# Kernel optimization log

Hardware: AMD Instinct MI355X
Metric: run time of the kernel (lower is better)

The kernel has to match this reference:

```python
import jax, jax.numpy as jnp
import numpy as np

VOCAB, H, HEADS, S, FF = 100, 8, 2, 6, 16
HD = H // HEADS  # head_dim = 4
EPS = 1e-5


def _layernorm(x, g, b):
    mu = jnp.mean(x, axis=-1, keepdims=True)
    var = jnp.mean((x - mu) ** 2, axis=-1, keepdims=True)
    return (x - mu) * jax.lax.rsqrt(var + EPS) * g + b


def setup_inputs() -> dict:
    key = jax.random.key(0)
    ks = jax.random.split(key, 20)
    B = 262144
    d = {
        'input_ids': jax.random.randint(ks[0], (B, S), 0, VOCAB),
        'tok_emb': jax.random.normal(ks[1], (VOCAB, H), jnp.float32) * 0.02,
        'pos_emb': jax.random.normal(ks[2], (S, H), jnp.float32) * 0.02,
        'Wq': jax.random.normal(ks[3], (H, H), jnp.float32) * 0.1,
        'bq': jnp.zeros((H,), jnp.float32),
        'Wk': jax.random.normal(ks[4], (H, H), jnp.float32) * 0.1,
        'bk': jnp.zeros((H,), jnp.float32),
        'Wv': jax.random.normal(ks[5], (H, H), jnp.float32) * 0.1,
        'bv': jnp.zeros((H,), jnp.float32),
        'Wo': jax.random.normal(ks[6], (H, H), jnp.float32) * 0.1,
        'bo': jnp.zeros((H,), jnp.float32),
        'W1': jax.random.normal(ks[7], (FF, H), jnp.float32) * 0.1,
        'b1': jnp.zeros((FF,), jnp.float32),
        'W2': jax.random.normal(ks[8], (H, FF), jnp.float32) * 0.1,
        'b2': jnp.zeros((H,), jnp.float32),
        'g1': jnp.ones((H,), jnp.float32),
        'be1': jnp.zeros((H,), jnp.float32),
        'g2': jnp.ones((H,), jnp.float32),
        'be2': jnp.zeros((H,), jnp.float32),
    }
    return d


def reference(input_ids, tok_emb, pos_emb, Wq, bq, Wk, bk, Wv, bv, Wo, bo,
              W1, b1, W2, b2, g1, be1, g2, be2):
    B, Sq = input_ids.shape
    x = tok_emb[input_ids] + pos_emb[None, :, :]  # [B,S,H]
    q = x @ Wq.T + bq
    k = x @ Wk.T + bk
    v = x @ Wv.T + bv
    # split heads: [B, heads, S, head_dim]
    q = q.reshape(B, Sq, HEADS, HD).transpose(0, 2, 1, 3)
    k = k.reshape(B, Sq, HEADS, HD).transpose(0, 2, 1, 3)
    v = v.reshape(B, Sq, HEADS, HD).transpose(0, 2, 1, 3)
    scores = jnp.einsum('bhsd,bhtd->bhst', q, k) / (HD ** 0.5)
    probs = jax.nn.softmax(scores, axis=-1)
    attn = jnp.einsum('bhst,bhtd->bhsd', probs, v)
    attn = attn.transpose(0, 2, 1, 3).reshape(B, Sq, H)
    attn = attn @ Wo.T + bo
    h = _layernorm(x + attn, g1, be1)
    ffn = jax.nn.gelu(h @ W1.T + b1, approximate=False) @ W2.T + b2
    return _layernorm(h + ffn, g2, be2)
```

## Files before the change

### kernel.cpp

```cpp
#include <hip/hip_runtime.h>

#define TT_S 6
#define TT_H 8
#define TT_FF 16

__global__ __launch_bounds__(256, 3) void tt_fused(
    const int* __restrict__ ids,
    const float* __restrict__ tok_emb, const float* __restrict__ pos_emb,
    const float* __restrict__ Wq, const float* __restrict__ bq,
    const float* __restrict__ Wk, const float* __restrict__ bk,
    const float* __restrict__ Wv, const float* __restrict__ bv,
    const float* __restrict__ Wo, const float* __restrict__ bo,
    const float* __restrict__ W1, const float* __restrict__ b1,
    const float* __restrict__ W2, const float* __restrict__ b2,
    const float* __restrict__ g1, const float* __restrict__ be1,
    const float* __restrict__ g2, const float* __restrict__ be2,
    float* __restrict__ out, int B)
{
  __shared__ __align__(16) float s_tok[800];
  const int tid = threadIdx.x;
  for (int i = tid; i < 800; i += 256) s_tok[i] = tok_emb[i];
  __syncthreads();

  const int b = blockIdx.x * 256 + tid;
  if (b >= B) return;

  const int* idp = ids + (size_t)b * TT_S;
  int2 i0 = *(const int2*)(idp + 0);
  int2 i1 = *(const int2*)(idp + 2);
  int2 i2 = *(const int2*)(idp + 4);
  unsigned long long P =
      (unsigned long long)(unsigned)i0.x        |
      ((unsigned long long)(unsigned)i0.y << 8) |
      ((unsigned long long)(unsigned)i1.x << 16)|
      ((unsigned long long)(unsigned)i1.y << 24)|
      ((unsigned long long)(unsigned)i2.x << 32)|
      ((unsigned long long)(unsigned)i2.y << 40);

  float km[TT_S][TT_H], vm[TT_S][TT_H];
  {
    float x[TT_S][TT_H];
    const int idv[TT_S] = { i0.x, i0.y, i1.x, i1.y, i2.x, i2.y };
    #pragma unroll
    for (int t = 0; t < TT_S; ++t) {
      const float4* tr = (const float4*)(s_tok + idv[t] * TT_H);
      float4 a0 = tr[0];
      float4 a1 = tr[1];
      x[t][0] = a0.x + pos_emb[t*8+0];
      x[t][1] = a0.y + pos_emb[t*8+1];
      x[t][2] = a0.z + pos_emb[t*8+2];
      x[t][3] = a0.w + pos_emb[t*8+3];
      x[t][4] = a1.x + pos_emb[t*8+4];
      x[t][5] = a1.y + pos_emb[t*8+5];
      x[t][6] = a1.z + pos_emb[t*8+6];
      x[t][7] = a1.w + pos_emb[t*8+7];
    }
    #pragma unroll
    for (int i = 0; i < TT_H; ++i) {
      float ak[TT_S], av[TT_S];
      float bki = bk[i], bvi = bv[i];
      #pragma unroll
      for (int t = 0; t < TT_S; ++t) { ak[t] = bki; av[t] = bvi; }
      #pragma unroll
      for (int j = 0; j < TT_H; ++j) {
        float wk = Wk[i*8+j], wv = Wv[i*8+j];
        #pragma unroll
        for (int t = 0; t < TT_S; ++t) {
          ak[t] = fmaf(x[t][j], wk, ak[t]);
          av[t] = fmaf(x[t][j], wv, av[t]);
        }
      }
      #pragma unroll
      for (int t = 0; t < TT_S; ++t) { km[t][i] = ak[t]; vm[t][i] = av[t]; }
    }
  }

  float* op = out + (size_t)b * (TT_S * TT_H);
  #pragma unroll 1
  for (int s = 0; s < TT_S; ++s) {
    const int tok = (int)((P >> (s * 8)) & 0xFF);
    const float4* xr = (const float4*)(s_tok + tok * TT_H);
    float4 a0 = xr[0];
    float4 a1 = xr[1];
    float xs[TT_H];
    xs[0] = a0.x + pos_emb[s*8+0];
    xs[1] = a0.y + pos_emb[s*8+1];
    xs[2] = a0.z + pos_emb[s*8+2];
    xs[3] = a0.w + pos_emb[s*8+3];
    xs[4] = a1.x + pos_emb[s*8+4];
    xs[5] = a1.y + pos_emb[s*8+5];
    xs[6] = a1.z + pos_emb[s*8+6];
    xs[7] = a1.w + pos_emb[s*8+7];

    float qs[TT_H];
    #pragma unroll
    for (int i = 0; i < TT_H; ++i) {
      float a = bq[i];
      #pragma unroll
      for (int j = 0; j < TT_H; ++j) a = fmaf(xs[j], Wq[i*8+j], a);
      qs[i] = a * 0.5f;
    }

    float attn[TT_H];
    #pragma unroll
    for (int hh = 0; hh < 2; ++hh) {
      const int hb = hh * 4;
      float sc[TT_S];
      float sum = 0.f;
      #pragma unroll
      for (int t = 0; t < TT_S; ++t) {
        float d = qs[hb+0] * km[t][hb+0];
        d = fmaf(qs[hb+1], km[t][hb+1], d);
        d = fmaf(qs[hb+2], km[t][hb+2], d);
        d = fmaf(qs[hb+3], km[t][hb+3], d);
        sc[t] = __expf(d);
        sum += sc[t];
      }
      float inv = __builtin_amdgcn_rcpf(sum);
      float a0_ = 0.f, a1_ = 0.f, a2_ = 0.f, a3_ = 0.f;
      #pragma unroll
      for (int t = 0; t < TT_S; ++t) {
        a0_ = fmaf(sc[t], vm[t][hb+0], a0_);
        a1_ = fmaf(sc[t], vm[t][hb+1], a1_);
        a2_ = fmaf(sc[t], vm[t][hb+2], a2_);
        a3_ = fmaf(sc[t], vm[t][hb+3], a3_);
      }
      attn[hb+0] = a0_ * inv;
      attn[hb+1] = a1_ * inv;
      attn[hb+2] = a2_ * inv;
      attn[hb+3] = a3_ * inv;
    }

    float r[TT_H];
    float mu = 0.f;
    #pragma unroll
    for (int i = 0; i < TT_H; ++i) {
      float o = bo[i];
      #pragma unroll
      for (int j = 0; j < TT_H; ++j) o = fmaf(attn[j], Wo[i*8+j], o);
      r[i] = xs[i] + o;
      mu += r[i];
    }
    mu *= 0.125f;
    float var = 0.f;
    #pragma unroll
    for (int i = 0; i < TT_H; ++i) { float d = r[i] - mu; var = fmaf(d, d, var); }
    var *= 0.125f;
    float rin = __builtin_amdgcn_rsqf(var + 1e-5f);
    float hr[TT_H];
    #pragma unroll
    for (int i = 0; i < TT_H; ++i)
      hr[i] = fmaf((r[i] - mu) * rin, g1[i], be1[i]);

    float f1[TT_FF];
    #pragma unroll
    for (int f = 0; f < TT_FF; ++f) {
      float u = b1[f];
      #pragma unroll
      for (int j = 0; j < TT_H; ++j) u = fmaf(hr[j], W1[f*8+j], u);
      float u2 = u * u;
      float p  = fmaf(0.044715f, u2, 1.0f);
      float z2 = fminf(1.5957691216057308f * u * p, 60.f);
      float e  = __expf(z2);
      f1[f] = u * e * __builtin_amdgcn_rcpf(e + 1.0f);
    }

    float r2[TT_H];
    float mu2 = 0.f;
    #pragma unroll
    for (int i = 0; i < TT_H; ++i) {
      float y = b2[i];
      #pragma unroll
      for (int f = 0; f < TT_FF; ++f) y = fmaf(f1[f], W2[i*16+f], y);
      r2[i] = hr[i] + y;
      mu2 += r2[i];
    }
    mu2 *= 0.125f;
    float var2 = 0.f;
    #pragma unroll
    for (int i = 0; i < TT_H; ++i) { float d = r2[i] - mu2; var2 = fmaf(d, d, var2); }
    var2 *= 0.125f;
    float rin2 = __builtin_amdgcn_rsqf(var2 + 1e-5f);
    float res[TT_H];
    #pragma unroll
    for (int i = 0; i < TT_H; ++i)
      res[i] = fmaf((r2[i] - mu2) * rin2, g2[i], be2[i]);

    float4 v0; v0.x = res[0]; v0.y = res[1]; v0.z = res[2]; v0.w = res[3];
    float4 v1; v1.x = res[4]; v1.y = res[5]; v1.z = res[6]; v1.w = res[7];
    ((float4*)(op + s*8))[0] = v0;
    ((float4*)(op + s*8))[1] = v1;
  }
}

extern "C" void kernel_launch(void* const* d_in, const int* in_sizes, int n_in,
                              void* d_out, int out_size, void* d_ws, size_t ws_size,
                              hipStream_t stream) {
  const int*   ids = (const int*)  d_in[0];
  const float* tok = (const float*)d_in[1];
  const float* pos = (const float*)d_in[2];
  const float* Wq  = (const float*)d_in[3];
  const float* bq  = (const float*)d_in[4];
  const float* Wk  = (const float*)d_in[5];
  const float* bk  = (const float*)d_in[6];
  const float* Wv  = (const float*)d_in[7];
  const float* bv  = (const float*)d_in[8];
  const float* Wo  = (const float*)d_in[9];
  const float* bo  = (const float*)d_in[10];
  const float* W1  = (const float*)d_in[11];
  const float* b1  = (const float*)d_in[12];
  const float* W2  = (const float*)d_in[13];
  const float* b2  = (const float*)d_in[14];
  const float* g1  = (const float*)d_in[15];
  const float* be1 = (const float*)d_in[16];
  const float* g2  = (const float*)d_in[17];
  const float* be2 = (const float*)d_in[18];
  float* out = (float*)d_out;

  const int B = in_sizes[0] / TT_S;
  const int grid = (B + 255) / 256;
  hipLaunchKernelGGL(tt_fused, dim3(grid), dim3(256), 0, stream,
                     ids, tok, pos, Wq, bq, Wk, bk, Wv, bv, Wo, bo,
                     W1, b1, W2, b2, g1, be1, g2, be2, out, B);
}
```

Baseline: 166.2 us.

## Map one thread per token and share K/V through LDS

Result: faster. 142.8 us (-14.1%).

```diff
diff --git a/kernel.cpp b/kernel.cpp
--- a/kernel.cpp
+++ b/kernel.cpp
@@ -3,8 +3,11 @@
 #define TT_S 6
 #define TT_H 8
 #define TT_FF 16
-
-__global__ __launch_bounds__(256, 3) void tt_fused(
+#define SEQ_PER_BLK 64
+#define BLK (SEQ_PER_BLK * TT_S)
+#define KV_STRIDE 108
+
+__global__ __launch_bounds__(BLK, 6) void tt_fused(
     const int* __restrict__ ids,
     const float* __restrict__ tok_emb, const float* __restrict__ pos_emb,
     const float* __restrict__ Wq, const float* __restrict__ bq,
@@ -18,178 +21,162 @@
     float* __restrict__ out, int B)
 {
   __shared__ __align__(16) float s_tok[800];
+  __shared__ __align__(16) float s_pos[48];
+  __shared__ __align__(16) float s_kv[SEQ_PER_BLK * KV_STRIDE];
+
   const int tid = threadIdx.x;
-  for (int i = tid; i < 800; i += 256) s_tok[i] = tok_emb[i];
+  for (int i = tid; i < 800; i += BLK) s_tok[i] = tok_emb[i];
+  if (tid < 48) s_pos[tid] = pos_emb[tid];
   __syncthreads();
 
-  const int b = blockIdx.x * 256 + tid;
-  if (b >= B) return;
-
-  const int* idp = ids + (size_t)b * TT_S;
-  int2 i0 = *(const int2*)(idp + 0);
-  int2 i1 = *(const int2*)(idp + 2);
-  int2 i2 = *(const int2*)(idp + 4);
-  unsigned long long P =
-      (unsigned long long)(unsigned)i0.x        |
-      ((unsigned long long)(unsigned)i0.y << 8) |
-      ((unsigned long long)(unsigned)i1.x << 16)|
-      ((unsigned long long)(unsigned)i1.y << 24)|
-      ((unsigned long long)(unsigned)i2.x << 32)|
-      ((unsigned long long)(unsigned)i2.y << 40);
-
-  float km[TT_S][TT_H], vm[TT_S][TT_H];
+  const int s_loc = tid / TT_S;
+  const int t     = tid - s_loc * TT_S;
+  const int seq_g = blockIdx.x * SEQ_PER_BLK + s_loc;
+  const bool valid = (seq_g < B);
+
+  const size_t gidx = (size_t)blockIdx.x * BLK + tid;
+  const int id = valid ? ids[gidx] : 0;
+
+  const float4* tr = (const float4*)(s_tok + id * TT_H);
+  float4 a0 = tr[0];
+  float4 a1 = tr[1];
+  const float4* pr = (const float4*)(s_pos + t * TT_H);
+  float4 p0 = pr[0];
+  float4 p1 = pr[1];
+  float xs[TT_H];
+  xs[0] = a0.x + p0.x; xs[1] = a0.y + p0.y; xs[2] = a0.z + p0.z; xs[3] = a0.w + p0.w;
+  xs[4] = a1.x + p1.x; xs[5] = a1.y + p1.y; xs[6] = a1.z + p1.z; xs[7] = a1.w + p1.w;
+
   {
-    float x[TT_S][TT_H];
-    const int idv[TT_S] = { i0.x, i0.y, i1.x, i1.y, i2.x, i2.y };
-    #pragma unroll
-    for (int t = 0; t < TT_S; ++t) {
-      const float4* tr = (const float4*)(s_tok + idv[t] * TT_H);
-      float4 a0 = tr[0];
-      float4 a1 = tr[1];
-      x[t][0] = a0.x + pos_emb[t*8+0];
-      x[t][1] = a0.y + pos_emb[t*8+1];
-      x[t][2] = a0.z + pos_emb[t*8+2];
-      x[t][3] = a0.w + pos_emb[t*8+3];
-      x[t][4] = a1.x + pos_emb[t*8+4];
-      x[t][5] = a1.y + pos_emb[t*8+5];
-      x[t][6] = a1.z + pos_emb[t*8+6];
-      x[t][7] = a1.w + pos_emb[t*8+7];
-    }
+    float kr[TT_H], vr[TT_H];
     #pragma unroll
     for (int i = 0; i < TT_H; ++i) {
-      float ak[TT_S], av[TT_S];
-      float bki = bk[i], bvi = bv[i];
-      #pragma unroll
-      for (int t = 0; t < TT_S; ++t) { ak[t] = bki; av[t] = bvi; }
+      float ak = bk[i], av = bv[i];
       #pragma unroll
       for (int j = 0; j < TT_H; ++j) {
-        float wk = Wk[i*8+j], wv = Wv[i*8+j];
-        #pragma unroll
-        for (int t = 0; t < TT_S; ++t) {
-          ak[t] = fmaf(x[t][j], wk, ak[t]);
-          av[t] = fmaf(x[t][j], wv, av[t]);
-        }
+        ak = fmaf(xs[j], Wk[i*8+j], ak);
+        av = fmaf(xs[j], Wv[i*8+j], av);
       }
-      #pragma unroll
-      for (int t = 0; t < TT_S; ++t) { km[t][i] = ak[t]; vm[t][i] = av[t]; }
+      kr[i] = ak; vr[i] = av;
     }
-  }
-
-  float* op = out + (size_t)b * (TT_S * TT_H);
-  #pragma unroll 1
-  for (int s = 0; s < TT_S; ++s) {
-    const int tok = (int)((P >> (s * 8)) & 0xFF);
-    const float4* xr = (const float4*)(s_tok + tok * TT_H);
-    float4 a0 = xr[0];
-    float4 a1 = xr[1];
-    float xs[TT_H];
-    xs[0] = a0.x + pos_emb[s*8+0];
-    xs[1] = a0.y + pos_emb[s*8+1];
-    xs[2] = a0.z + pos_emb[s*8+2];
-    xs[3] = a0.w + pos_emb[s*8+3];
-    xs[4] = a1.x + pos_emb[s*8+4];
-    xs[5] = a1.y + pos_emb[s*8+5];
-    xs[6] = a1.z + pos_emb[s*8+6];
-    xs[7] = a1.w + pos_emb[s*8+7];
-
-    float qs[TT_H];
-    #pragma unroll
-    for (int i = 0; i < TT_H; ++i) {
-      float a = bq[i];
-      #pragma unroll
-      for (int j = 0; j < TT_H; ++j) a = fmaf(xs[j], Wq[i*8+j], a);
-      qs[i] = a * 0.5f;
-    }
-
-    float attn[TT_H];
-    #pragma unroll
-    for (int hh = 0; hh < 2; ++hh) {
-      const int hb = hh * 4;
-      float sc[TT_S];
-      float sum = 0.f;
-      #pragma unroll
-      for (int t = 0; t < TT_S; ++t) {
-        float d = qs[hb+0] * km[t][hb+0];
-        d = fmaf(qs[hb+1], km[t][hb+1], d);
-        d = fmaf(qs[hb+2], km[t][hb+2], d);
-        d = fmaf(qs[hb+3], km[t][hb+3], d);
-        sc[t] = __expf(d);
-        sum += sc[t];
-      }
-      float inv = __builtin_amdgcn_rcpf(sum);
-      float a0_ = 0.f, a1_ = 0.f, a2_ = 0.f, a3_ = 0.f;
-      #pragma unroll
-      for (int t = 0; t < TT_S; ++t) {
-        a0_ = fmaf(sc[t], vm[t][hb+0], a0_);
-        a1_ = fmaf(sc[t], vm[t][hb+1], a1_);
-        a2_ = fmaf(sc[t], vm[t][hb+2], a2_);
-        a3_ = fmaf(sc[t], vm[t][hb+3], a3_);
-      }
-      attn[hb+0] = a0_ * inv;
-      attn[hb+1] = a1_ * inv;
-      attn[hb+2] = a2_ * inv;
-      attn[hb+3] = a3_ * inv;
-    }
-
-    float r[TT_H];
-    float mu = 0.f;
-    #pragma unroll
-    for (int i = 0; i < TT_H; ++i) {
-      float o = bo[i];
-      #pragma unroll
-      for (int j = 0; j < TT_H; ++j) o = fmaf(attn[j], Wo[i*8+j], o);
-      r[i] = xs[i] + o;
-      mu += r[i];
-    }
-    mu *= 0.125f;
-    float var = 0.f;
-    #pragma unroll
-    for (int i = 0; i < TT_H; ++i) { float d = r[i] - mu; var = fmaf(d, d, var); }
-    var *= 0.125f;
-    float rin = __builtin_amdgcn_rsqf(var + 1e-5f);
-    float hr[TT_H];
-    #pragma unroll
-    for (int i = 0; i < TT_H; ++i)
-      hr[i] = fmaf((r[i] - mu) * rin, g1[i], be1[i]);
-
-    float f1[TT_FF];
-    #pragma unroll
-    for (int f = 0; f < TT_FF; ++f) {
-      float u = b1[f];
-      #pragma unroll
-      for (int j = 0; j < TT_H; ++j) u = fmaf(hr[j], W1[f*8+j], u);
-      float u2 = u * u;
-      float p  = fmaf(0.044715f, u2, 1.0f);
-      float z2 = fminf(1.5957691216057308f * u * p, 60.f);
-      float e  = __expf(z2);
-      f1[f] = u * e * __builtin_amdgcn_rcpf(e + 1.0f);
-    }
-
-    float r2[TT_H];
-    float mu2 = 0.f;
-    #pragma unroll
-    for (int i = 0; i < TT_H; ++i) {
-      float y = b2[i];
-      #pragma unroll
-      for (int f = 0; f < TT_FF; ++f) y = fmaf(f1[f], W2[i*16+f], y);
-      r2[i] = hr[i] + y;
-      mu2 += r2[i];
-    }
-    mu2 *= 0.125f;
-    float var2 = 0.f;
-    #pragma unroll
-    for (int i = 0; i < TT_H; ++i) { float d = r2[i] - mu2; var2 = fmaf(d, d, var2); }
-    var2 *= 0.125f;
-    float rin2 = __builtin_amdgcn_rsqf(var2 + 1e-5f);
-    float res[TT_H];
-    #pragma unroll
-    for (int i = 0; i < TT_H; ++i)
-      res[i] = fmaf((r2[i] - mu2) * rin2, g2[i], be2[i]);
-
+    float* kvp = s_kv + s_loc * KV_STRIDE + t * 16;
+    float4 w0; w0.x = kr[0]; w0.y = kr[1]; w0.z = kr[2]; w0.w = kr[3];
+    float4 w1; w1.x = kr[4]; w1.y = kr[5]; w1.z = kr[6]; w1.w = kr[7];
+    float4 w2; w2.x = vr[0]; w2.y = vr[1]; w2.z = vr[2]; w2.w = vr[3];
+    float4 w3; w3.x = vr[4]; w3.y = vr[5]; w3.z = vr[6]; w3.w = vr[7];
+    ((float4*)kvp)[0] = w0;
+    ((float4*)kvp)[1] = w1;
+    ((float4*)kvp)[2] = w2;
+    ((float4*)kvp)[3] = w3;
+  }
+  __syncthreads();
+
+  float qs[TT_H];
+  #pragma unroll
+  for (int i = 0; i < TT_H; ++i) {
+    float a = bq[i];
+    #pragma unroll
+    for (int j = 0; j < TT_H; ++j) a = fmaf(xs[j], Wq[i*8+j], a);
+    qs[i] = a * 0.5f;
+  }
+
+  float acc[TT_H] = {0.f,0.f,0.f,0.f,0.f,0.f,0.f,0.f};
+  float sum0 = 0.f, sum1 = 0.f;
+  const float4* kvb = (const float4*)(s_kv + s_loc * KV_STRIDE);
+  #pragma unroll
+  for (int t2 = 0; t2 < TT_S; ++t2) {
+    float4 ka = kvb[t2*4+0];
+    float4 kb = kvb[t2*4+1];
+    float4 va = kvb[t2*4+2];
+    float4 vb = kvb[t2*4+3];
+    float d0 = qs[0]*ka.x;
+    d0 = fmaf(qs[1], ka.y, d0);
+    d0 = fmaf(qs[2], ka.z, d0);
+    d0 = fmaf(qs[3], ka.w, d0);
+    float d1 = qs[4]*kb.x;
+    d1 = fmaf(qs[5], kb.y, d1);
+    d1 = fmaf(qs[6], kb.z, d1);
+    d1 = fmaf(qs[7], kb.w, d1);
+    float e0 = __expf(d0);
+    float e1 = __expf(d1);
+    sum0 += e0; sum1 += e1;
+    acc[0] = fmaf(e0, va.x, acc[0]);
+    acc[1] = fmaf(e0, va.y, acc[1]);
+    acc[2] = fmaf(e0, va.z, acc[2]);
+    acc[3] = fmaf(e0, va.w, acc[3]);
+    acc[4] = fmaf(e1, vb.x, acc[4]);
+    acc[5] = fmaf(e1, vb.y, acc[5]);
+    acc[6] = fmaf(e1, vb.z, acc[6]);
+    acc[7] = fmaf(e1, vb.w, acc[7]);
+  }
+  {
+    float inv0 = __builtin_amdgcn_rcpf(sum0);
+    float inv1 = __builtin_amdgcn_rcpf(sum1);
+    acc[0] *= inv0; acc[1] *= inv0; acc[2] *= inv0; acc[3] *= inv0;
+    acc[4] *= inv1; acc[5] *= inv1; acc[6] *= inv1; acc[7] *= inv1;
+  }
+
+  float r[TT_H];
+  float mu = 0.f;
+  #pragma unroll
+  for (int i = 0; i < TT_H; ++i) {
+    float o = bo[i];
+    #pragma unroll
+    for (int j = 0; j < TT_H; ++j) o = fmaf(acc[j], Wo[i*8+j], o);
+    r[i] = xs[i] + o;
+    mu += r[i];
+  }
+  mu *= 0.125f;
+  float var = 0.f;
+  #pragma unroll
+  for (int i = 0; i < TT_H; ++i) { float d = r[i] - mu; var = fmaf(d, d, var); }
+  var *= 0.125f;
+  float rin = __builtin_amdgcn_rsqf(var + 1e-5f);
+  float hr[TT_H];
+  #pragma unroll
+  for (int i = 0; i < TT_H; ++i)
+    hr[i] = fmaf((r[i] - mu) * rin, g1[i], be1[i]);
+
+  float f1[TT_FF];
+  #pragma unroll
+  for (int f = 0; f < TT_FF; ++f) {
+    float u = b1[f];
+    #pragma unroll
+    for (int j = 0; j < TT_H; ++j) u = fmaf(hr[j], W1[f*8+j], u);
+    float u2 = u * u;
+    float p  = fmaf(0.044715f, u2, 1.0f);
+    float z2 = fminf(1.5957691216057308f * u * p, 60.f);
+    float e  = __expf(z2);
+    f1[f] = u * e * __builtin_amdgcn_rcpf(e + 1.0f);
+  }
+
+  float r2[TT_H];
+  float mu2 = 0.f;
+  #pragma unroll
+  for (int i = 0; i < TT_H; ++i) {
+    float y = b2[i];
+    #pragma unroll
+    for (int f = 0; f < TT_FF; ++f) y = fmaf(f1[f], W2[i*16+f], y);
+    r2[i] = hr[i] + y;
+    mu2 += r2[i];
+  }
+  mu2 *= 0.125f;
+  float var2 = 0.f;
+  #pragma unroll
+  for (int i = 0; i < TT_H; ++i) { float d = r2[i] - mu2; var2 = fmaf(d, d, var2); }
+  var2 *= 0.125f;
+  float rin2 = __builtin_amdgcn_rsqf(var2 + 1e-5f);
+  float res[TT_H];
+  #pragma unroll
+  for (int i = 0; i < TT_H; ++i)
+    res[i] = fmaf((r2[i] - mu2) * rin2, g2[i], be2[i]);
+
+  if (valid) {
+    float* op = out + gidx * TT_H;
     float4 v0; v0.x = res[0]; v0.y = res[1]; v0.z = res[2]; v0.w = res[3];
     float4 v1; v1.x = res[4]; v1.y = res[5]; v1.z = res[6]; v1.w = res[7];
-    ((float4*)(op + s*8))[0] = v0;
-    ((float4*)(op + s*8))[1] = v1;
+    ((float4*)op)[0] = v0;
+    ((float4*)op)[1] = v1;
   }
 }
 
@@ -218,8 +205,8 @@
   float* out = (float*)d_out;
 
   const int B = in_sizes[0] / TT_S;
-  const int grid = (B + 255) / 256;
-  hipLaunchKernelGGL(tt_fused, dim3(grid), dim3(256), 0, stream,
+  const int grid = (B + SEQ_PER_BLK - 1) / SEQ_PER_BLK;
+  hipLaunchKernelGGL(tt_fused, dim3(grid), dim3(BLK), 0, stream,
                      ids, tok, pos, Wq, bq, Wk, bk, Wv, bv, Wo, bo,
                      W1, b1, W2, b2, g1, be1, g2, be2, out, B);
 }
```
